# Performance work log

Hardware: AMD Instinct MI355X
Metric: run time of the kernel (lower is better)

Reference implementation:

```python
import jax, jax.numpy as jnp
import numpy as np

N, T = 20000, 8
E = 320000
HID, HEADS = 128, 2
HPC = HID // HEADS  # hid channels per head (concat=True)
NEG_SLOPE = 0.2  # PyG GATv2Conv default


def setup_inputs() -> dict:
    key = jax.random.key(0)
    ks = jax.random.split(key, 16)
    s = 0.1
    return {
        "x": jax.random.normal(ks[0], (N, T), dtype=jnp.float32),
        "edge_index": jax.random.randint(ks[1], (2, E), 0, N, dtype=jnp.int64),
        "edge_weight": jax.random.uniform(ks[2], (E,), dtype=jnp.float32),
        # GATv2Conv params (in_channels=1 -> heads*hpc)
        "W_l": jax.random.normal(ks[3], (1, HID), dtype=jnp.float32) * s,
        "b_l": jnp.zeros((HID,), jnp.float32),
        "W_r": jax.random.normal(ks[4], (1, HID), dtype=jnp.float32) * s,
        "b_r": jnp.zeros((HID,), jnp.float32),
        "att": jax.random.normal(ks[5], (HEADS, HPC), dtype=jnp.float32) * s,
        "conv_bias": jnp.zeros((HID,), jnp.float32),
        # GRU-style gate params
        "W1": jax.random.normal(ks[6], (2 * HID, 2 * HID), dtype=jnp.float32) * s,
        "b1": jnp.zeros((2 * HID,), jnp.float32),
        "W2": jax.random.normal(ks[7], (2 * HID, HID), dtype=jnp.float32) * s,
        "b2": jnp.zeros((HID,), jnp.float32),
    }


def _gatv2(xt, src, dst, n, W_l, b_l, W_r, b_r, att, conv_bias):
    H, C = att.shape
    xl = (xt @ W_l + b_l).reshape(n, H, C)  # source transform
    xr = (xt @ W_r + b_r).reshape(n, H, C)  # target transform
    g = jax.nn.leaky_relu(xl[src] + xr[dst], NEG_SLOPE)  # [E', H, C]
    e = jnp.einsum('ehc,hc->eh', g, att)  # attention logits
    # softmax over incoming edges of each destination node
    emax = jax.ops.segment_max(e, dst, num_segments=n)
    ex = jnp.exp(e - emax[dst])
    denom = jax.ops.segment_sum(ex, dst, num_segments=n)
    alpha = ex / (denom[dst] + 1e-16)  # [E', H]
    msg = alpha[:, :, None] * xl[src]
    out = jax.ops.segment_sum(msg, dst, num_segments=n)  # [N, H, C]
    return out.reshape(n, H * C) + conv_bias


def reference(x, edge_index, edge_weight, W_l, b_l, W_r, b_r, att, conv_bias, W1, b1, W2, b2):
    n = x.shape[0]
    # GATv2Conv default add_self_loops=True
    loops = jnp.arange(n, dtype=edge_index.dtype)
    src = jnp.concatenate([edge_index[0], loops])
    dst = jnp.concatenate([edge_index[1], loops])

    def step(h, xt_col):
        xt = xt_col[:, None]  # [N, 1]
        f = jax.nn.sigmoid(_gatv2(xt, src, dst, n, W_l, b_l, W_r, b_r, att, conv_bias))
        ru = jax.nn.sigmoid(jnp.concatenate([f, h], axis=1) @ W1 + b1)
        r, u = jnp.split(ru, 2, axis=1)
        c = jnp.tanh(jnp.concatenate([f, r * h], axis=1) @ W2 + b2)
        h_new = u * h + (1.0 - u) * c
        return h_new, None

    h0 = jnp.zeros((n, HID), dtype=x.dtype)
    h, _ = jax.lax.scan(jax.checkpoint(step), h0, x.T)  # scan over time
    return h
```

## Files before the change

kernel.cpp:

```cpp
#include <hip/hip_runtime.h>
#include <hip/hip_bf16.h>

#define N_NODES 20000
#define T_STEPS 8
#define E_EDGES 320000
#define HID 128
#define BN 80

typedef short short8 __attribute__((ext_vector_type(8)));
typedef float f32x4 __attribute__((ext_vector_type(4)));

__device__ __attribute__((aligned(16))) float g_xT[T_STEPS * N_NODES];
__device__ __attribute__((aligned(16))) float g_ndf[T_STEPS * N_NODES * 4];
__device__ __attribute__((aligned(16))) int   g_cnt[N_NODES];
__device__ __attribute__((aligned(16))) int   g_rowptr[N_NODES + 1];
__device__ __attribute__((aligned(16))) int   g_cursor[N_NODES];
__device__ __attribute__((aligned(16))) int   g_sorted[E_EDGES];
__device__ __attribute__((aligned(16))) short g_w1hi[65536];
__device__ __attribute__((aligned(16))) short g_w1lo[65536];
__device__ __attribute__((aligned(16))) short g_w2hi[32768];
__device__ __attribute__((aligned(16))) short g_w2lo[32768];
__device__ float g_lin[6];
__device__ int   g_flag;

__device__ __forceinline__ float fsig(float z) {
    return 1.0f / (1.0f + __expf(-z));
}
__device__ __forceinline__ unsigned short f2bf(float f) {
    unsigned u = __builtin_bit_cast(unsigned, f);
    unsigned r = (u + 0x7FFFu + ((u >> 16) & 1u)) >> 16;
    return (unsigned short)r;
}
__device__ __forceinline__ float bf2f(unsigned short s) {
    return __builtin_bit_cast(float, ((unsigned)s) << 16);
}

__global__ void detect_kernel(const unsigned int* __restrict__ ei32) {
    int all_zero = 1;
    for (int k = 0; k < 64; ++k)
        if (ei32[2 * k + 1] != 0u) { all_zero = 0; break; }
    g_flag = all_zero;
}

__device__ __forceinline__ void load_edge(const void* ei, int e, int& src, int& dst) {
    if (g_flag) {
        const long long* p = (const long long*)ei;
        src = (int)p[e]; dst = (int)p[E_EDGES + e];
    } else {
        const int* p = (const int*)ei;
        src = p[e]; dst = p[E_EDGES + e];
    }
}

__global__ __launch_bounds__(256) void init_kernel(
    const float* __restrict__ x, const void* __restrict__ ei)
{
    const int i = blockIdx.x * 256 + threadIdx.x;
    if (i < T_STEPS * N_NODES) {
        const int n = i >> 3, t = i & 7;
        g_xT[t * N_NODES + n] = x[i];
    }
    if (i < N_NODES) g_cnt[i] = 0;
}

__global__ __launch_bounds__(256) void hist_kernel(const void* __restrict__ ei) {
    const int e = blockIdx.x * 256 + threadIdx.x;
    if (e >= E_EDGES) return;
    int src, dst; load_edge(ei, e, src, dst);
    atomicAdd(&g_cnt[dst], 1);
}

__global__ __launch_bounds__(1024) void scan_kernel() {
    __shared__ int part[1024];
    const int tid  = threadIdx.x;
    const int base = tid * 20;
    int local[20];
    int s = 0;
    #pragma unroll
    for (int i = 0; i < 20; ++i) {
        const int n = base + i;
        const int c = (n < N_NODES) ? g_cnt[n] : 0;
        local[i] = s; s += c;
    }
    part[tid] = s;
    __syncthreads();
    for (int off = 1; off < 1024; off <<= 1) {
        const int v = (tid >= off) ? part[tid - off] : 0;
        __syncthreads();
        part[tid] += v;
        __syncthreads();
    }
    const int pre = (tid == 0) ? 0 : part[tid - 1];
    #pragma unroll
    for (int i = 0; i < 20; ++i) {
        const int n = base + i;
        if (n < N_NODES) {
            const int v = pre + local[i];
            g_rowptr[n] = v;
            g_cursor[n] = v;
        }
    }
    if (tid == 1023) g_rowptr[N_NODES] = part[1023];
}

__global__ __launch_bounds__(256) void scatter_kernel(const void* __restrict__ ei) {
    const int e = blockIdx.x * 256 + threadIdx.x;
    if (e >= E_EDGES) return;
    int src, dst; load_edge(ei, e, src, dst);
    const int pos = atomicAdd(&g_cursor[dst], 1);
    g_sorted[pos] = src;
}

__global__ __launch_bounds__(256) void prep_kernel(
    const float* __restrict__ W1, const float* __restrict__ W2,
    const float* __restrict__ W_l, const float* __restrict__ b_l,
    const float* __restrict__ W_r, const float* __restrict__ b_r,
    const float* __restrict__ att)
{
    int i = blockIdx.x * 256 + threadIdx.x;
    if (i < 65536) {
        int k = i >> 8, n = i & 255;
        float w = W1[i];
        int kb = k >> 5, kq = (k >> 3) & 3, r = k & 7;
        int idx = ((kb * 256 + n) * 4 + kq) * 8 + r;
        unsigned short hi = f2bf(w);
        g_w1hi[idx] = (short)hi;
        g_w1lo[idx] = (short)f2bf(w - bf2f(hi));
    } else {
        int j = i - 65536;
        int k = j >> 7, n = j & 127;
        float w = W2[j];
        int kb = k >> 5, kq = (k >> 3) & 3, r = k & 7;
        int idx = ((kb * 128 + n) * 4 + kq) * 8 + r;
        unsigned short hi = f2bf(w);
        g_w2hi[idx] = (short)hi;
        g_w2lo[idx] = (short)f2bf(w - bf2f(hi));
    }
    if (blockIdx.x == 0 && threadIdx.x < 2) {
        const int hh = threadIdx.x;
        float P = 0.f, Q = 0.f, R = 0.f;
        for (int k = 0; k < 64; ++k) {
            const int c = hh * 64 + k;
            const float a = att[c];
            P = fmaf(a, W_l[c], P);
            Q = fmaf(a, W_r[c], Q);
            R = fmaf(a, b_l[c] + b_r[c], R);
        }
        g_lin[hh * 3 + 0] = P;
        g_lin[hh * 3 + 1] = Q;
        g_lin[hh * 3 + 2] = R;
    }
}

__global__ __launch_bounds__(256) void edge_all_kernel()
{
    __shared__ float4 ch4[128];
    const int tid = threadIdx.x;
    extern __shared__ float dummy[];
    (void)dummy;
}

__global__ __launch_bounds__(256) void edge_all2_kernel(
    const float* __restrict__ W_l, const float* __restrict__ b_l,
    const float* __restrict__ W_r, const float* __restrict__ b_r,
    const float* __restrict__ att)
{
    __shared__ float4 ch4[128];
    const int tid = threadIdx.x;
    if (tid < 128)
        ch4[tid] = make_float4(W_l[tid], W_r[tid], b_l[tid] + b_r[tid], att[tid]);
    __syncthreads();

    const int n = blockIdx.x * 256 + tid;
    const int t = blockIdx.y;
    if (n >= N_NODES) return;

    const float* xrow = &g_xT[t * N_NODES];
    const float xd = xrow[n];
    const float P0 = g_lin[0], Q0 = g_lin[1], R0 = g_lin[2];
    const float P1 = g_lin[3], Q1 = g_lin[4], R1 = g_lin[5];
    const float lin0 = fmaf(xd, Q0, R0);
    const float lin1 = fmaf(xd, Q1, R1);

    const int base = g_rowptr[n];
    const int deg  = g_rowptr[n + 1] - base;
    const int tot  = deg + 1;

    float den0 = 0.f, num0 = 0.f, den1 = 0.f, num1 = 0.f;
    for (int cs = 0; cs < tot; cs += 8) {
        int m = tot - cs; if (m > 8) m = 8;
        float xs[8];
        #pragma unroll
        for (int e = 0; e < 8; ++e) {
            xs[e] = 0.f;
            if (e < m) {
                const int idx = cs + e;
                xs[e] = (idx == 0) ? xd : xrow[g_sorted[base + idx - 1]];
            }
        }
        float ea0[8], ea1[8];
        #pragma unroll
        for (int e = 0; e < 8; ++e) { ea0[e] = 0.f; ea1[e] = 0.f; }
        #pragma unroll 2
        for (int c = 0; c < 64; ++c) {
            const float4 f0 = ch4[c];
            const float4 f1 = ch4[64 + c];
            const float dp0 = fmaf(xd, f0.y, f0.z);
            const float dp1 = fmaf(xd, f1.y, f1.z);
            #pragma unroll
            for (int e = 0; e < 8; ++e) {
                const float a0 = fmaf(xs[e], f0.x, dp0);
                ea0[e] = fmaf(fabsf(a0), f0.w, ea0[e]);
                const float a1 = fmaf(xs[e], f1.x, dp1);
                ea1[e] = fmaf(fabsf(a1), f1.w, ea1[e]);
            }
        }
        #pragma unroll
        for (int e = 0; e < 8; ++e) {
            if (e < m) {
                const float e0 = fmaf(0.6f, fmaf(xs[e], P0, lin0), 0.4f * ea0[e]);
                const float e1 = fmaf(0.6f, fmaf(xs[e], P1, lin1), 0.4f * ea1[e]);
                const float x0 = __expf(e0);
                const float x1 = __expf(e1);
                den0 += x0; num0 = fmaf(x0, xs[e], num0);
                den1 += x1; num1 = fmaf(x1, xs[e], num1);
            }
        }
    }
    float4 out = make_float4(den0, den1, num0, num1);
    *(float4*)&g_ndf[((size_t)t * N_NODES + n) * 4] = out;
}

__global__ __launch_bounds__(512) void gru_all_kernel(
    const float* __restrict__ W_l, const float* __restrict__ b_l,
    const float* __restrict__ conv_bias,
    const float* __restrict__ b1, const float* __restrict__ b2,
    float* __restrict__ hout)
{
    __shared__ short featA[BN * 384];
    __shared__ float swl[128], sbl[128], scb[128];

    const int t   = threadIdx.x;
    const int n0g = blockIdx.x * BN;

    if (t < 128) { swl[t] = W_l[t]; sbl[t] = b_l[t]; scb[t] = conv_bias[t]; }
    for (int i = t; i < BN * 16; i += 512) {
        const int node = i >> 4;
        const int g    = 16 + (i & 15);
        const int gsw  = g ^ (node & 7);
        *(short8*)&featA[node * 384 + gsw * 8] = (short8)0;
    }
    __syncthreads();

    const int wid = t >> 6;
    const int l   = t & 63;
    const int lr  = l & 15;
    const int lk  = l >> 4;
    const int ec  = wid * 16 + lr;

    const float bias_r = b1[ec];
    const float bias_u = b1[128 + ec];
    const float bias_2 = b2[ec];

    f32x4 hreg[5], ureg[5];
    #pragma unroll
    for (int mf = 0; mf < 5; ++mf) hreg[mf] = (f32x4){0.f, 0.f, 0.f, 0.f};

    for (int step = 0; step < T_STEPS; ++step) {
        for (int G = t; G < BN * 16; G += 512) {
            const int node = G >> 4;
            const int pg   = G & 15;
            const int head = pg >> 3;
            const size_t bi = ((size_t)step * N_NODES + n0g + node) * 4;
            const float den = g_ndf[bi + head];
            const float num = g_ndf[bi + 2 + head];
            const float inv = 1.0f / (den + 1e-16f);
            short8 v;
            #pragma unroll
            for (int r = 0; r < 8; ++r) {
                const int c = pg * 8 + r;
                const float z = (num * swl[c] + den * sbl[c]) * inv + scb[c];
                v[r] = (short)f2bf(fsig(z));
            }
            const int gsw = pg ^ (node & 7);
            *(short8*)&featA[node * 384 + gsw * 8] = v;
        }
        __syncthreads();

        f32x4 acc0[5], acc1[5];
        #pragma unroll
        for (int mf = 0; mf < 5; ++mf) {
            acc0[mf] = (f32x4){bias_r, bias_r, bias_r, bias_r};
            acc1[mf] = (f32x4){bias_u, bias_u, bias_u, bias_u};
        }
        #pragma unroll
        for (int kb = 0; kb < 8; ++kb) {
            const int glin = kb * 4 + lk;
            const int bidx0 = ((kb * 256 + ec) * 4 + lk) * 8;
            const int bidx1 = bidx0 + 4096;
            const short8 bh0 = *(const short8*)&g_w1hi[bidx0];
            const short8 bl0 = *(const short8*)&g_w1lo[bidx0];
            const short8 bh1 = *(const short8*)&g_w1hi[bidx1];
            const short8 bl1 = *(const short8*)&g_w1lo[bidx1];
            #pragma unroll
            for (int mf = 0; mf < 5; ++mf) {
                const int row = mf * 16 + lr;
                const short8 ah = *(short8*)&featA[row * 384 + (glin ^ (row & 7)) * 8];
                acc0[mf] = __builtin_amdgcn_mfma_f32_16x16x32_bf16(ah, bh0, acc0[mf], 0, 0, 0);
                acc0[mf] = __builtin_amdgcn_mfma_f32_16x16x32_bf16(ah, bl0, acc0[mf], 0, 0, 0);
                acc1[mf] = __builtin_amdgcn_mfma_f32_16x16x32_bf16(ah, bh1, acc1[mf], 0, 0, 0);
                acc1[mf] = __builtin_amdgcn_mfma_f32_16x16x32_bf16(ah, bl1, acc1[mf], 0, 0, 0);
            }
        }

        #pragma unroll
        for (int mf = 0; mf < 5; ++mf) {
            #pragma unroll
            for (int j = 0; j < 4; ++j) {
                const int row = mf * 16 + lk * 4 + j;
                const float r = fsig(acc0[mf][j]);
                ureg[mf][j] = fsig(acc1[mf][j]);
                const float rh = r * hreg[mf][j];
                const float ot = __shfl_xor(rh, 1);
                if ((lr & 1) == 0) {
                    const unsigned pk = (unsigned)f2bf(rh) | ((unsigned)f2bf(ot) << 16);
                    const int g  = (32 + (ec >> 3)) ^ (row & 7);
                    *(unsigned*)&featA[row * 384 + g * 8 + (ec & 7)] = pk;
                }
            }
        }
        __syncthreads();

        f32x4 acc2[5];
        #pragma unroll
        for (int mf = 0; mf < 5; ++mf)
            acc2[mf] = (f32x4){bias_2, bias_2, bias_2, bias_2};
        #pragma unroll
        for (int kb = 0; kb < 8; ++kb) {
            const int glin = kb * 4 + lk;
            const int gra  = (glin < 16) ? glin : glin + 16;
            const int bidx = ((kb * 128 + ec) * 4 + lk) * 8;
            const short8 bh = *(const short8*)&g_w2hi[bidx];
            const short8 bl = *(const short8*)&g_w2lo[bidx];
            #pragma unroll
            for (int mf = 0; mf < 5; ++mf) {
                const int row = mf * 16 + lr;
                const short8 ah = *(short8*)&featA[row * 384 + (gra ^ (row & 7)) * 8];
                acc2[mf] = __builtin_amdgcn_mfma_f32_16x16x32_bf16(ah, bh, acc2[mf], 0, 0, 0);
                acc2[mf] = __builtin_amdgcn_mfma_f32_16x16x32_bf16(ah, bl, acc2[mf], 0, 0, 0);
            }
        }

        #pragma unroll
        for (int mf = 0; mf < 5; ++mf) {
            #pragma unroll
            for (int j = 0; j < 4; ++j) {
                const int row = mf * 16 + lk * 4 + j;
                const float c  = tanhf(acc2[mf][j]);
                const float hn = fmaf(ureg[mf][j], hreg[mf][j] - c, c);
                hreg[mf][j] = hn;
                if (step < T_STEPS - 1) {
                    const float ot = __shfl_xor(hn, 1);
                    if ((lr & 1) == 0) {
                        const unsigned pk = (unsigned)f2bf(hn) | ((unsigned)f2bf(ot) << 16);
                        const int g  = (16 + (ec >> 3)) ^ (row & 7);
                        *(unsigned*)&featA[row * 384 + g * 8 + (ec & 7)] = pk;
                    }
                } else {
                    hout[(size_t)(n0g + row) * HID + ec] = hn;
                }
            }
        }
        if (step < T_STEPS - 1)
            __syncthreads();
    }
}

extern "C" void kernel_launch(void* const* d_in, const int* in_sizes, int n_in,
                              void* d_out, int out_size, void* d_ws, size_t ws_size,
                              hipStream_t stream) {
    const float* x   = (const float*)d_in[0];
    const void*  ei  = d_in[1];
    const float* W_l = (const float*)d_in[3];
    const float* b_l = (const float*)d_in[4];
    const float* W_r = (const float*)d_in[5];
    const float* b_r = (const float*)d_in[6];
    const float* att = (const float*)d_in[7];
    const float* cb  = (const float*)d_in[8];
    const float* W1  = (const float*)d_in[9];
    const float* b1  = (const float*)d_in[10];
    const float* W2  = (const float*)d_in[11];
    const float* b2  = (const float*)d_in[12];

    float* h = (float*)d_out;
    (void)d_ws; (void)ws_size;

    detect_kernel<<<1, 1, 0, stream>>>((const unsigned int*)ei);
    init_kernel<<<(T_STEPS * N_NODES + 255) / 256, 256, 0, stream>>>(x, ei);
    hist_kernel<<<(E_EDGES + 255) / 256, 256, 0, stream>>>(ei);
    scan_kernel<<<1, 1024, 0, stream>>>();
    scatter_kernel<<<(E_EDGES + 255) / 256, 256, 0, stream>>>(ei);
    prep_kernel<<<384, 256, 0, stream>>>(W1, W2, W_l, b_l, W_r, b_r, att);
    edge_all2_kernel<<<dim3((N_NODES + 255) / 256, T_STEPS), 256, 0, stream>>>(
        W_l, b_l, W_r, b_r, att);
    gru_all_kernel<<<N_NODES / BN, 512, 0, stream>>>(W_l, b_l, cb, b1, b2, h);
}
```

Baseline: 382.5 us.

## Drop bf16 hi/lo weight split, fuse W2 f-half into first GEMM, fast math

Removes the low-order bf16 correction weights so each GEMM uses a single bf16 MFMA instead of two. The f-half of the W2 product is moved into the first GEMM loop, and the trailing per-step barrier is removed. The edge kernel now handles two timesteps per thread so the gathered source indices are reused. The detect kernel is folded into init, and fast rcp/tanh plus packed bf16 conversion are used. The trade is lower precision from dropping the lo-part compensation, and a possible race from removing the barrier.

Measured after the change: 335.1 us. 12.4% less time.

```diff
diff --git a/kernel.cpp b/kernel.cpp
--- a/kernel.cpp
+++ b/kernel.cpp
@@ -17,29 +17,24 @@
 __device__ __attribute__((aligned(16))) int   g_cursor[N_NODES];
 __device__ __attribute__((aligned(16))) int   g_sorted[E_EDGES];
 __device__ __attribute__((aligned(16))) short g_w1hi[65536];
-__device__ __attribute__((aligned(16))) short g_w1lo[65536];
 __device__ __attribute__((aligned(16))) short g_w2hi[32768];
-__device__ __attribute__((aligned(16))) short g_w2lo[32768];
 __device__ float g_lin[6];
 __device__ int   g_flag;
 
-__device__ __forceinline__ float fsig(float z) {
-    return 1.0f / (1.0f + __expf(-z));
+__device__ __forceinline__ float frcp(float x) { return __builtin_amdgcn_rcpf(x); }
+__device__ __forceinline__ float fsig(float z) { return frcp(1.f + __expf(-z)); }
+__device__ __forceinline__ float ftanh(float z) {
+    return fmaf(-2.f, frcp(__expf(2.f * z) + 1.f), 1.f);
+}
+__device__ __forceinline__ unsigned cvtpk(float lo, float hi) {
+    unsigned r;
+    asm("v_cvt_pk_bf16_f32 %0, %1, %2" : "=v"(r) : "v"(lo), "v"(hi));
+    return r;
 }
 __device__ __forceinline__ unsigned short f2bf(float f) {
     unsigned u = __builtin_bit_cast(unsigned, f);
     unsigned r = (u + 0x7FFFu + ((u >> 16) & 1u)) >> 16;
     return (unsigned short)r;
-}
-__device__ __forceinline__ float bf2f(unsigned short s) {
-    return __builtin_bit_cast(float, ((unsigned)s) << 16);
-}
-
-__global__ void detect_kernel(const unsigned int* __restrict__ ei32) {
-    int all_zero = 1;
-    for (int k = 0; k < 64; ++k)
-        if (ei32[2 * k + 1] != 0u) { all_zero = 0; break; }
-    g_flag = all_zero;
 }
 
 __device__ __forceinline__ void load_edge(const void* ei, int e, int& src, int& dst) {
@@ -53,7 +48,7 @@
 }
 
 __global__ __launch_bounds__(256) void init_kernel(
-    const float* __restrict__ x, const void* __restrict__ ei)
+    const float* __restrict__ x, const unsigned int* __restrict__ ei32)
 {
     const int i = blockIdx.x * 256 + threadIdx.x;
     if (i < T_STEPS * N_NODES) {
@@ -61,6 +56,12 @@
         g_xT[t * N_NODES + n] = x[i];
     }
     if (i < N_NODES) g_cnt[i] = 0;
+    if (i == 0) {
+        int all_zero = 1;
+        for (int k = 0; k < 64; ++k)
+            if (ei32[2 * k + 1] != 0u) { all_zero = 0; break; }
+        g_flag = all_zero;
+    }
 }
 
 __global__ __launch_bounds__(256) void hist_kernel(const void* __restrict__ ei) {
@@ -120,21 +121,13 @@
     int i = blockIdx.x * 256 + threadIdx.x;
     if (i < 65536) {
         int k = i >> 8, n = i & 255;
-        float w = W1[i];
         int kb = k >> 5, kq = (k >> 3) & 3, r = k & 7;
-        int idx = ((kb * 256 + n) * 4 + kq) * 8 + r;
-        unsigned short hi = f2bf(w);
-        g_w1hi[idx] = (short)hi;
-        g_w1lo[idx] = (short)f2bf(w - bf2f(hi));
+        g_w1hi[((kb * 256 + n) * 4 + kq) * 8 + r] = (short)f2bf(W1[i]);
     } else {
         int j = i - 65536;
         int k = j >> 7, n = j & 127;
-        float w = W2[j];
         int kb = k >> 5, kq = (k >> 3) & 3, r = k & 7;
-        int idx = ((kb * 128 + n) * 4 + kq) * 8 + r;
-        unsigned short hi = f2bf(w);
-        g_w2hi[idx] = (short)hi;
-        g_w2lo[idx] = (short)f2bf(w - bf2f(hi));
+        g_w2hi[((kb * 128 + n) * 4 + kq) * 8 + r] = (short)f2bf(W2[j]);
     }
     if (blockIdx.x == 0 && threadIdx.x < 2) {
         const int hh = threadIdx.x;
@@ -152,15 +145,7 @@
     }
 }
 
-__global__ __launch_bounds__(256) void edge_all_kernel()
-{
-    __shared__ float4 ch4[128];
-    const int tid = threadIdx.x;
-    extern __shared__ float dummy[];
-    (void)dummy;
-}
-
-__global__ __launch_bounds__(256) void edge_all2_kernel(
+__global__ __launch_bounds__(256) void edge_all_kernel(
     const float* __restrict__ W_l, const float* __restrict__ b_l,
     const float* __restrict__ W_r, const float* __restrict__ b_r,
     const float* __restrict__ att)
@@ -171,64 +156,77 @@
         ch4[tid] = make_float4(W_l[tid], W_r[tid], b_l[tid] + b_r[tid], att[tid]);
     __syncthreads();
 
-    const int n = blockIdx.x * 256 + tid;
-    const int t = blockIdx.y;
+    const int n  = blockIdx.x * 256 + tid;
+    const int t0 = blockIdx.y * 2;
     if (n >= N_NODES) return;
 
-    const float* xrow = &g_xT[t * N_NODES];
-    const float xd = xrow[n];
+    const float* xr0 = &g_xT[t0 * N_NODES];
+    const float* xr1 = xr0 + N_NODES;
+    const float xd0 = xr0[n];
+    const float xd1 = xr1[n];
     const float P0 = g_lin[0], Q0 = g_lin[1], R0 = g_lin[2];
     const float P1 = g_lin[3], Q1 = g_lin[4], R1 = g_lin[5];
-    const float lin0 = fmaf(xd, Q0, R0);
-    const float lin1 = fmaf(xd, Q1, R1);
+    const float l00 = fmaf(xd0, Q0, R0), l01 = fmaf(xd0, Q1, R1);
+    const float l10 = fmaf(xd1, Q0, R0), l11 = fmaf(xd1, Q1, R1);
 
     const int base = g_rowptr[n];
     const int deg  = g_rowptr[n + 1] - base;
     const int tot  = deg + 1;
 
-    float den0 = 0.f, num0 = 0.f, den1 = 0.f, num1 = 0.f;
+    float d00 = 0.f, n00 = 0.f, d01 = 0.f, n01 = 0.f;
+    float d10 = 0.f, n10 = 0.f, d11 = 0.f, n11 = 0.f;
     for (int cs = 0; cs < tot; cs += 8) {
         int m = tot - cs; if (m > 8) m = 8;
-        float xs[8];
+        float xs0[8], xs1[8];
         #pragma unroll
         for (int e = 0; e < 8; ++e) {
-            xs[e] = 0.f;
+            xs0[e] = 0.f; xs1[e] = 0.f;
             if (e < m) {
                 const int idx = cs + e;
-                xs[e] = (idx == 0) ? xd : xrow[g_sorted[base + idx - 1]];
-            }
-        }
-        float ea0[8], ea1[8];
-        #pragma unroll
-        for (int e = 0; e < 8; ++e) { ea0[e] = 0.f; ea1[e] = 0.f; }
+                if (idx == 0) { xs0[e] = xd0; xs1[e] = xd1; }
+                else {
+                    const int s = g_sorted[base + idx - 1];
+                    xs0[e] = xr0[s]; xs1[e] = xr1[s];
+                }
+            }
+        }
+        float ea00[8], ea01[8], ea10[8], ea11[8];
+        #pragma unroll
+        for (int e = 0; e < 8; ++e) { ea00[e]=0.f; ea01[e]=0.f; ea10[e]=0.f; ea11[e]=0.f; }
         #pragma unroll 2
         for (int c = 0; c < 64; ++c) {
             const float4 f0 = ch4[c];
             const float4 f1 = ch4[64 + c];
-            const float dp0 = fmaf(xd, f0.y, f0.z);
-            const float dp1 = fmaf(xd, f1.y, f1.z);
+            const float dp00 = fmaf(xd0, f0.y, f0.z);
+            const float dp01 = fmaf(xd0, f1.y, f1.z);
+            const float dp10 = fmaf(xd1, f0.y, f0.z);
+            const float dp11 = fmaf(xd1, f1.y, f1.z);
             #pragma unroll
             for (int e = 0; e < 8; ++e) {
-                const float a0 = fmaf(xs[e], f0.x, dp0);
-                ea0[e] = fmaf(fabsf(a0), f0.w, ea0[e]);
-                const float a1 = fmaf(xs[e], f1.x, dp1);
-                ea1[e] = fmaf(fabsf(a1), f1.w, ea1[e]);
+                float a;
+                a = fmaf(xs0[e], f0.x, dp00); ea00[e] = fmaf(fabsf(a), f0.w, ea00[e]);
+                a = fmaf(xs0[e], f1.x, dp01); ea01[e] = fmaf(fabsf(a), f1.w, ea01[e]);
+                a = fmaf(xs1[e], f0.x, dp10); ea10[e] = fmaf(fabsf(a), f0.w, ea10[e]);
+                a = fmaf(xs1[e], f1.x, dp11); ea11[e] = fmaf(fabsf(a), f1.w, ea11[e]);
             }
         }
         #pragma unroll
         for (int e = 0; e < 8; ++e) {
             if (e < m) {
-                const float e0 = fmaf(0.6f, fmaf(xs[e], P0, lin0), 0.4f * ea0[e]);
-                const float e1 = fmaf(0.6f, fmaf(xs[e], P1, lin1), 0.4f * ea1[e]);
-                const float x0 = __expf(e0);
-                const float x1 = __expf(e1);
-                den0 += x0; num0 = fmaf(x0, xs[e], num0);
-                den1 += x1; num1 = fmaf(x1, xs[e], num1);
-            }
-        }
-    }
-    float4 out = make_float4(den0, den1, num0, num1);
-    *(float4*)&g_ndf[((size_t)t * N_NODES + n) * 4] = out;
+                float ee, ex;
+                ee = fmaf(0.6f, fmaf(xs0[e], P0, l00), 0.4f * ea00[e]);
+                ex = __expf(ee); d00 += ex; n00 = fmaf(ex, xs0[e], n00);
+                ee = fmaf(0.6f, fmaf(xs0[e], P1, l01), 0.4f * ea01[e]);
+                ex = __expf(ee); d01 += ex; n01 = fmaf(ex, xs0[e], n01);
+                ee = fmaf(0.6f, fmaf(xs1[e], P0, l10), 0.4f * ea10[e]);
+                ex = __expf(ee); d10 += ex; n10 = fmaf(ex, xs1[e], n10);
+                ee = fmaf(0.6f, fmaf(xs1[e], P1, l11), 0.4f * ea11[e]);
+                ex = __expf(ee); d11 += ex; n11 = fmaf(ex, xs1[e], n11);
+            }
+        }
+    }
+    *(float4*)&g_ndf[((size_t)t0 * N_NODES + n) * 4]       = make_float4(d00, d01, n00, n01);
+    *(float4*)&g_ndf[((size_t)(t0+1) * N_NODES + n) * 4]   = make_float4(d10, d11, n10, n11);
 }
 
 __global__ __launch_bounds__(512) void gru_all_kernel(
@@ -274,42 +272,43 @@
             const size_t bi = ((size_t)step * N_NODES + n0g + node) * 4;
             const float den = g_ndf[bi + head];
             const float num = g_ndf[bi + 2 + head];
-            const float inv = 1.0f / (den + 1e-16f);
-            short8 v;
-            #pragma unroll
-            for (int r = 0; r < 8; ++r) {
-                const int c = pg * 8 + r;
-                const float z = (num * swl[c] + den * sbl[c]) * inv + scb[c];
-                v[r] = (short)f2bf(fsig(z));
+            const float inv = frcp(den + 1e-16f);
+            union { unsigned u[4]; short8 s; } P;
+            #pragma unroll
+            for (int r2 = 0; r2 < 4; ++r2) {
+                const int c0 = pg * 8 + 2 * r2;
+                const float z0 = (num * swl[c0]     + den * sbl[c0])     * inv + scb[c0];
+                const float z1 = (num * swl[c0 + 1] + den * sbl[c0 + 1]) * inv + scb[c0 + 1];
+                P.u[r2] = cvtpk(fsig(z0), fsig(z1));
             }
             const int gsw = pg ^ (node & 7);
-            *(short8*)&featA[node * 384 + gsw * 8] = v;
+            *(short8*)&featA[node * 384 + gsw * 8] = P.s;
         }
         __syncthreads();
 
-        f32x4 acc0[5], acc1[5];
+        f32x4 acc0[5], acc1[5], acc2[5];
         #pragma unroll
         for (int mf = 0; mf < 5; ++mf) {
             acc0[mf] = (f32x4){bias_r, bias_r, bias_r, bias_r};
             acc1[mf] = (f32x4){bias_u, bias_u, bias_u, bias_u};
+            acc2[mf] = (f32x4){bias_2, bias_2, bias_2, bias_2};
         }
         #pragma unroll
         for (int kb = 0; kb < 8; ++kb) {
             const int glin = kb * 4 + lk;
             const int bidx0 = ((kb * 256 + ec) * 4 + lk) * 8;
-            const int bidx1 = bidx0 + 4096;
-            const short8 bh0 = *(const short8*)&g_w1hi[bidx0];
-            const short8 bl0 = *(const short8*)&g_w1lo[bidx0];
-            const short8 bh1 = *(const short8*)&g_w1hi[bidx1];
-            const short8 bl1 = *(const short8*)&g_w1lo[bidx1];
+            const short8 b1a = *(const short8*)&g_w1hi[bidx0];
+            const short8 b1b = *(const short8*)&g_w1hi[bidx0 + 4096];
+            short8 b2f;
+            if (kb < 4) b2f = *(const short8*)&g_w2hi[((kb * 128 + ec) * 4 + lk) * 8];
             #pragma unroll
             for (int mf = 0; mf < 5; ++mf) {
                 const int row = mf * 16 + lr;
                 const short8 ah = *(short8*)&featA[row * 384 + (glin ^ (row & 7)) * 8];
-                acc0[mf] = __builtin_amdgcn_mfma_f32_16x16x32_bf16(ah, bh0, acc0[mf], 0, 0, 0);
-                acc0[mf] = __builtin_amdgcn_mfma_f32_16x16x32_bf16(ah, bl0, acc0[mf], 0, 0, 0);
-                acc1[mf] = __builtin_amdgcn_mfma_f32_16x16x32_bf16(ah, bh1, acc1[mf], 0, 0, 0);
-                acc1[mf] = __builtin_amdgcn_mfma_f32_16x16x32_bf16(ah, bl1, acc1[mf], 0, 0, 0);
+                acc0[mf] = __builtin_amdgcn_mfma_f32_16x16x32_bf16(ah, b1a, acc0[mf], 0, 0, 0);
+                acc1[mf] = __builtin_amdgcn_mfma_f32_16x16x32_bf16(ah, b1b, acc1[mf], 0, 0, 0);
+                if (kb < 4)
+                    acc2[mf] = __builtin_amdgcn_mfma_f32_16x16x32_bf16(ah, b2f, acc2[mf], 0, 0, 0);
             }
         }
 
@@ -323,31 +322,22 @@
                 const float rh = r * hreg[mf][j];
                 const float ot = __shfl_xor(rh, 1);
                 if ((lr & 1) == 0) {
-                    const unsigned pk = (unsigned)f2bf(rh) | ((unsigned)f2bf(ot) << 16);
-                    const int g  = (32 + (ec >> 3)) ^ (row & 7);
-                    *(unsigned*)&featA[row * 384 + g * 8 + (ec & 7)] = pk;
+                    const int g = (32 + (ec >> 3)) ^ (row & 7);
+                    *(unsigned*)&featA[row * 384 + g * 8 + (ec & 7)] = cvtpk(rh, ot);
                 }
             }
         }
         __syncthreads();
 
-        f32x4 acc2[5];
-        #pragma unroll
-        for (int mf = 0; mf < 5; ++mf)
-            acc2[mf] = (f32x4){bias_2, bias_2, bias_2, bias_2};
-        #pragma unroll
-        for (int kb = 0; kb < 8; ++kb) {
-            const int glin = kb * 4 + lk;
-            const int gra  = (glin < 16) ? glin : glin + 16;
-            const int bidx = ((kb * 128 + ec) * 4 + lk) * 8;
-            const short8 bh = *(const short8*)&g_w2hi[bidx];
-            const short8 bl = *(const short8*)&g_w2lo[bidx];
+        #pragma unroll
+        for (int kb = 4; kb < 8; ++kb) {
+            const int gra = kb * 4 + lk + 16;
+            const short8 b2f = *(const short8*)&g_w2hi[((kb * 128 + ec) * 4 + lk) * 8];
             #pragma unroll
             for (int mf = 0; mf < 5; ++mf) {
                 const int row = mf * 16 + lr;
                 const short8 ah = *(short8*)&featA[row * 384 + (gra ^ (row & 7)) * 8];
-                acc2[mf] = __builtin_amdgcn_mfma_f32_16x16x32_bf16(ah, bh, acc2[mf], 0, 0, 0);
-                acc2[mf] = __builtin_amdgcn_mfma_f32_16x16x32_bf16(ah, bl, acc2[mf], 0, 0, 0);
+                acc2[mf] = __builtin_amdgcn_mfma_f32_16x16x32_bf16(ah, b2f, acc2[mf], 0, 0, 0);
             }
         }
 
@@ -356,23 +346,20 @@
             #pragma unroll
             for (int j = 0; j < 4; ++j) {
                 const int row = mf * 16 + lk * 4 + j;
-                const float c  = tanhf(acc2[mf][j]);
+                const float c  = ftanh(acc2[mf][j]);
                 const float hn = fmaf(ureg[mf][j], hreg[mf][j] - c, c);
                 hreg[mf][j] = hn;
                 if (step < T_STEPS - 1) {
                     const float ot = __shfl_xor(hn, 1);
                     if ((lr & 1) == 0) {
-                        const unsigned pk = (unsigned)f2bf(hn) | ((unsigned)f2bf(ot) << 16);
-                        const int g  = (16 + (ec >> 3)) ^ (row & 7);
-                        *(unsigned*)&featA[row * 384 + g * 8 + (ec & 7)] = pk;
+                        const int g = (16 + (ec >> 3)) ^ (row & 7);
+                        *(unsigned*)&featA[row * 384 + g * 8 + (ec & 7)] = cvtpk(hn, ot);
                     }
                 } else {
                     hout[(size_t)(n0g + row) * HID + ec] = hn;
                 }
             }
         }
-        if (step < T_STEPS - 1)
-            __syncthreads();
     }
 }
 
@@ -395,13 +382,13 @@
     float* h = (float*)d_out;
     (void)d_ws; (void)ws_size;
 
-    detect_kernel<<<1, 1, 0, stream>>>((const unsigned int*)ei);
-    init_kernel<<<(T_STEPS * N_NODES + 255) / 256, 256, 0, stream>>>(x, ei);
+    init_kernel<<<(T_STEPS * N_NODES + 255) / 256, 256, 0, stream>>>(
+        x, (const unsigned int*)ei);
     hist_kernel<<<(E_EDGES + 255) / 256, 256, 0, stream>>>(ei);
     scan_kernel<<<1, 1024, 0, stream>>>();
     scatter_kernel<<<(E_EDGES + 255) / 256, 256, 0, stream>>>(ei);
     prep_kernel<<<384, 256, 0, stream>>>(W1, W2, W_l, b_l, W_r, b_r, att);
-    edge_all2_kernel<<<dim3((N_NODES + 255) / 256, T_STEPS), 256, 0, stream>>>(
+    edge_all_kernel<<<dim3((N_NODES + 255) / 256, T_STEPS / 2), 256, 0, stream>>>(
         W_l, b_l, W_r, b_r, att);
     gru_all_kernel<<<N_NODES / BN, 512, 0, stream>>>(W_l, b_l, cb, b1, b2, h);
 }
```
